# Kernel optimization log

Hardware: AMD Instinct MI355X
Metric: run time of the kernel (lower is better)

Reference implementation:

```python
import jax, jax.numpy as jnp
import numpy as np

N = 100000       # nodes
E = 1600000      # edges (avg degree 16)
F_IN = 128
F_OUT = 128
EPS = 1e-5       # GraphNorm eps
NEG_SLOPE = 0.01 # nn.LeakyReLU default


def setup_inputs() -> dict:
    key = jax.random.key(0)
    ks = jax.random.split(key, 4)
    x = jax.random.normal(ks[0], (N, F_IN), dtype=jnp.float32)
    edge_index = jax.random.randint(ks[1], (2, E), 0, N, dtype=jnp.int64)
    # GCNConv linear weight (stored as [in, out] for x @ W)
    W = jax.random.normal(ks[2], (F_IN, F_OUT), dtype=jnp.float32) / np.sqrt(F_IN).astype(np.float32)
    b = jnp.zeros((F_OUT,), jnp.float32)          # GCNConv bias
    gn_weight = jnp.ones((F_OUT,), jnp.float32)   # GraphNorm weight
    gn_bias = jnp.zeros((F_OUT,), jnp.float32)    # GraphNorm bias
    gn_mean_scale = jnp.ones((F_OUT,), jnp.float32)  # GraphNorm mean_scale
    return {"x": x, "edge_index": edge_index, "W": W, "b": b,
            "gn_weight": gn_weight, "gn_bias": gn_bias, "gn_mean_scale": gn_mean_scale}


def reference(x, edge_index, W, b, gn_weight, gn_bias, gn_mean_scale):
    n = x.shape[0]
    # --- GCNConv with add_self_loops=True, symmetric normalization ---
    loops = jnp.arange(n, dtype=edge_index.dtype)
    src = jnp.concatenate([edge_index[0], loops])  # [E+N]
    dst = jnp.concatenate([edge_index[1], loops])  # [E+N]
    deg = jax.ops.segment_sum(jnp.ones(src.shape, x.dtype), dst, num_segments=n)  # [N]
    deg_inv_sqrt = jnp.where(deg > 0, 1.0 / jnp.sqrt(deg), 0.0)
    norm = deg_inv_sqrt[src] * deg_inv_sqrt[dst]   # [E+N]
    h = x @ W                                      # [N, F_OUT]
    agg = jax.ops.segment_sum(h[src] * norm[:, None], dst, num_segments=n) + b  # [N, F_OUT]
    # --- GraphNorm (single graph: stats over all nodes, per-feature) ---
    mean = jnp.mean(agg, axis=0)                   # [F_OUT]
    centered = agg - mean * gn_mean_scale
    var = jnp.mean(centered * centered, axis=0)
    out = centered / jnp.sqrt(var + EPS) * gn_weight + gn_bias
    # --- LeakyReLU ---
    out = jnp.where(out > 0, out, NEG_SLOPE * out)
    return (out, edge_index)
```

## Files before the change

### kernel.cpp

```cpp
#include <hip/hip_runtime.h>

#define NN 100000
#define NE 1600000
#define F  128
#define NSPL 50000

#define SH   8
#define NPB  256
#define NBKT 391
#define B1   256
#define CH1  6250
#define MATN (NBKT * B1)
#define MATP (98 * 1024)
#define BCAP2 6144

#define SB   256

constexpr float EPS   = 1e-5f;
constexpr float SLOPE = 0.01f;

typedef __attribute__((ext_vector_type(8))) short short8;
typedef __attribute__((ext_vector_type(4))) float f32x4;
typedef __attribute__((ext_vector_type(2))) float f32x2;

__device__ inline unsigned int bf16rne(float f) {
    unsigned int u = __float_as_uint(f);
    return (u + 0x7fffu + ((u >> 16) & 1u)) >> 16;
}
__device__ inline float blo(unsigned int u) { return __uint_as_float(u << 16); }
__device__ inline float bhi(unsigned int u) { return __uint_as_float(u & 0xffff0000u); }
__device__ inline unsigned int pack2(float a, float b) {
    return bf16rne(a) | (bf16rne(b) << 16);
}
__device__ inline f32x2 pkadd(f32x2 a, f32x2 b) {
    f32x2 d;
    asm("v_pk_add_f32 %0, %1, %2" : "=v"(d) : "v"(a), "v"(b));
    return d;
}
__device__ inline f32x2 fp8lo(unsigned int u) {
    return __builtin_amdgcn_cvt_pk_f32_fp8(u, false);
}
__device__ inline f32x2 fp8hi(unsigned int u) {
    return __builtin_amdgcn_cvt_pk_f32_fp8(u, true);
}
__device__ inline unsigned int fp8pack4(float a, float b, float c, float d) {
    int o = 0;
    o = __builtin_amdgcn_cvt_pk_fp8_f32(a, b, o, false);
    o = __builtin_amdgcn_cvt_pk_fp8_f32(c, d, o, true);
    return (unsigned int)o;
}

__global__ __launch_bounds__(1024) void k_hist1(const int* __restrict__ dst,
                                                unsigned int* __restrict__ mat,
                                                const float* __restrict__ Wm,
                                                unsigned int* __restrict__ Wt) {
    __shared__ unsigned int h[NBKT];
    if (threadIdx.x < NBKT) h[threadIdx.x] = 0u;
    __syncthreads();
    if (blockIdx.x < 8) {
        int idx = blockIdx.x * 1024 + threadIdx.x;
        int p = idx & 3, lane = (idx >> 2) & 63, n = (idx >> 8) & 7, kk = idx >> 11;
        int k0 = kk * 32 + (lane >> 4) * 8 + 2 * p;
        int c  = n * 16 + (lane & 15);
        unsigned int lo = bf16rne(Wm[k0 * F + c]);
        unsigned int hi = bf16rne(Wm[(k0 + 1) * F + c]);
        Wt[idx] = lo | (hi << 16);
    }
    const int e0 = blockIdx.x * CH1;
    for (int i = threadIdx.x; i < CH1; i += 1024)
        atomicAdd(&h[dst[e0 + i] >> SH], 1u);
    __syncthreads();
    if (threadIdx.x < NBKT) mat[threadIdx.x * B1 + blockIdx.x] = h[threadIdx.x];
}

__global__ __launch_bounds__(1024) void k_scanA(const unsigned int* __restrict__ mat,
                                                unsigned int* __restrict__ scn,
                                                unsigned int* __restrict__ bsums) {
    __shared__ unsigned int ps[1024];
    const int t = threadIdx.x;
    const int i = blockIdx.x * 1024 + t;
    unsigned int v = mat[i];
    ps[t] = v;
    __syncthreads();
    for (int off = 1; off < 1024; off <<= 1) {
        unsigned int a = (t >= off) ? ps[t - off] : 0u;
        __syncthreads();
        ps[t] += a;
        __syncthreads();
    }
    scn[i] = ps[t];
    if (t == 1023) bsums[blockIdx.x] = ps[1023];
}


__global__ __launch_bounds__(1024) void k_scat1(const int* __restrict__ ei,
                                                const unsigned int* __restrict__ mat,
                                                const unsigned int* __restrict__ scn,
                                                const unsigned int* __restrict__ bsums,
                                                unsigned int* __restrict__ ebuf) {
    __shared__ unsigned int cur[NBKT];
    __shared__ unsigned int bo[128];
    const int t = threadIdx.x;
    if (t < 128) {
        unsigned int v = (t < 98) ? bsums[t] : 0u;
        bo[t] = v;
        for (int off = 1; off < 128; off <<= 1) {
            __syncthreads();
            unsigned int a = (t >= off) ? bo[t - off] : 0u;
            __syncthreads();
            bo[t] += a;
        }
        bo[t] -= v;
    } else {
        for (int off = 1; off < 128; off <<= 1) { __syncthreads(); __syncthreads(); }
    }
    __syncthreads();
    if (t < NBKT) {
        int idx = t * B1 + blockIdx.x;
        cur[t] = scn[idx] + bo[idx >> 10] - mat[idx];
    }
    __syncthreads();
    const int e0 = blockIdx.x * CH1;
    for (int i = t; i < CH1; i += 1024) {
        int s = ei[e0 + i];
        int d = ei[NE + e0 + i];
        unsigned int pos = atomicAdd(&cur[d >> SH], 1u);
        ebuf[pos] = ((unsigned int)(d & (NPB - 1)) << 17) | (unsigned int)s;
    }
}

__global__ __launch_bounds__(256) void k_fill2(const unsigned int* __restrict__ mat,
                                               const unsigned int* __restrict__ scn,
                                               const unsigned int* __restrict__ bsums,
                                               const unsigned int* __restrict__ ebuf,
                                               int* __restrict__ row_start,
                                               float* __restrict__ dis,
                                               int* __restrict__ csr) {
    __shared__ unsigned int stage[BCAP2];
    __shared__ unsigned int hist[NPB];
    __shared__ unsigned int cur[NPB];
    __shared__ unsigned int ps[NPB];
    __shared__ unsigned int bo[128];
    const int t = threadIdx.x;
    const int bkt = blockIdx.x;
    hist[t] = 0u;
    if (t < 128) {
        unsigned int v = (t < 98) ? bsums[t] : 0u;
        bo[t] = v;
        for (int off = 1; off < 128; off <<= 1) {
            __syncthreads();
            unsigned int a = (t >= off) ? bo[t - off] : 0u;
            __syncthreads();
            bo[t] += a;
        }
        bo[t] -= v;
    } else {
        for (int off = 1; off < 128; off <<= 1) { __syncthreads(); __syncthreads(); }
    }
    __syncthreads();
    const int i0 = bkt * B1;
    const unsigned int ebase = scn[i0] + bo[i0 >> 10] - mat[i0];
    unsigned int eend;
    if (bkt == NBKT - 1) eend = (unsigned int)NE;
    else {
        const int i1 = (bkt + 1) * B1;
        eend = scn[i1] + bo[i1 >> 10] - mat[i1];
    }
    const unsigned int n = eend - ebase;
    const unsigned int m = (n < BCAP2) ? n : BCAP2;
    for (unsigned int i = t; i < m; i += 256) {
        unsigned int v = ebuf[ebase + i];
        stage[i] = v;
        atomicAdd(&hist[v >> 17], 1u);
    }
    for (unsigned int i = BCAP2 + t; i < n; i += 256)
        atomicAdd(&hist[ebuf[ebase + i] >> 17], 1u);
    __syncthreads();
    const unsigned int deg = hist[t];
    ps[t] = deg;
    __syncthreads();
    for (int off = 1; off < 256; off <<= 1) {
        unsigned int a = (t >= off) ? ps[t - off] : 0u;
        __syncthreads();
        ps[t] += a;
        __syncthreads();
    }
    const unsigned int ex = (t == 0) ? 0u : ps[t - 1];
    cur[t] = ebase + ex;
    const int node = bkt * NPB + t;
    if (node <= NN) row_start[node] = (int)(ebase + ex);
    if (node < NN)  dis[node] = rsqrtf((float)(deg + 1u));
    __syncthreads();
    for (unsigned int i = t; i < m; i += 256) {
        unsigned int v = stage[i];
        unsigned int pos = atomicAdd(&cur[v >> 17], 1u);
        csr[pos] = (int)(v & 0x1FFFFu);
    }
    for (unsigned int i = BCAP2 + t; i < n; i += 256) {
        unsigned int v = ebuf[ebase + i];
        unsigned int pos = atomicAdd(&cur[v >> 17], 1u);
        csr[pos] = (int)(v & 0x1FFFFu);
    }
}

__global__ __launch_bounds__(256) void k_gemm(const float* __restrict__ x,
                                              const unsigned int* __restrict__ Wt,
                                              const float* __restrict__ dis,
                                              unsigned int* __restrict__ g32) {
    __shared__ unsigned int xl[128 * 64];
    const int tid = threadIdx.x;
    const int lane = tid & 63, wave = tid >> 6;
    const int row0 = blockIdx.x * 128;

#pragma unroll
    for (int i = 0; i < 16; ++i) {
        int fi = i * 256 + tid;
        int lr = fi >> 5;
        int cf = (fi & 31) * 4;
        int gr = row0 + lr; if (gr >= NN) gr = NN - 1;
        float4 v = *(const float4*)(x + (size_t)gr * F + cf);
        unsigned int u0 = pack2(v.x, v.y);
        unsigned int u1 = pack2(v.z, v.w);
        int cu = (cf >> 1) ^ ((lr & 7) << 2);
        uint2 w2; w2.x = u0; w2.y = u1;
        *(uint2*)&xl[lr * 64 + cu] = w2;
    }
    __syncthreads();

    const int rbase = row0 + wave * 32;
    short8 afr[2][4];
#pragma unroll
    for (int m = 0; m < 2; ++m) {
        int lr = wave * 32 + m * 16 + (lane & 15);
#pragma unroll
        for (int kk = 0; kk < 4; ++kk) {
            int cu = (kk * 16 + (lane >> 4) * 4) ^ ((lr & 7) << 2);
            afr[m][kk] = *(const short8*)&xl[lr * 64 + cu];
        }
    }

    f32x4 acc[2][8];
#pragma unroll
    for (int m = 0; m < 2; ++m)
#pragma unroll
        for (int n = 0; n < 8; ++n) { f32x4 z = {0.f, 0.f, 0.f, 0.f}; acc[m][n] = z; }

    const uint4* Wt4 = (const uint4*)Wt;
#pragma unroll
    for (int kk = 0; kk < 4; ++kk) {
        union { uint4 u; short8 s; } bfr[8];
#pragma unroll
        for (int n = 0; n < 8; ++n) bfr[n].u = Wt4[(kk * 8 + n) * 64 + lane];
#pragma unroll
        for (int m = 0; m < 2; ++m)
#pragma unroll
            for (int n = 0; n < 8; ++n)
                acc[m][n] = __builtin_amdgcn_mfma_f32_16x16x32_bf16(bfr[n].s, afr[m][kk], acc[m][n], 0, 0, 0);
    }

#pragma unroll
    for (int m = 0; m < 2; ++m) {
        int xr = rbase + m * 16 + (lane & 15);
        bool ok = xr < NN;
        float d = ok ? dis[xr] : 0.0f;
        unsigned int* gp = g32 + (size_t)(ok ? xr : 0) * 32 + (lane >> 4);
#pragma unroll
        for (int n = 0; n < 8; ++n) {
            unsigned int w = fp8pack4(acc[m][n][0] * d, acc[m][n][1] * d,
                                      acc[m][n][2] * d, acc[m][n][3] * d);
            if (ok) gp[n * 4] = w;
        }
    }
}

__global__ __launch_bounds__(256) void k_gather(const unsigned int* __restrict__ g32,
                                                const int* __restrict__ csr,
                                                const int* __restrict__ row_start,
                                                const float* __restrict__ dis,
                                                const float* __restrict__ b,
                                                unsigned int* __restrict__ agg_lo,
                                                unsigned int* __restrict__ agg_hi) {
    const int lane = threadIdx.x & 63;
    const int node = blockIdx.x * 4 + (threadIdx.x >> 6);
    if (node >= NN) return;
    const int q = lane >> 4;
    const int c = lane & 15;
    const int j = row_start[node];
    const int e = row_start[node + 1];
    const int L = e - j + 1;
    int sv = (j + lane < e) ? csr[j + lane] : node;
    f32x2 A0 = {0.f, 0.f}, A1 = A0, A2 = A0, A3 = A0;
    int k = 0;
    const int L1 = (L < 64) ? L : 64;
    for (; k < L1; k += 16) {
        int k0 = k + q, k1 = k0 + 4, k2 = k0 + 8, k3 = k0 + 12;
        int r0 = __shfl(sv, k0);
        int r1 = __shfl(sv, k1);
        int r2 = __shfl(sv, k2);
        int r3 = __shfl(sv, k3);
        bool p0 = k0 < L, p1 = k1 < L, p2 = k2 < L, p3 = k3 < L;
        uint2 v0, v1, v2, v3;
        if (p0) v0 = *(const uint2*)&g32[(size_t)r0 * 32 + c * 2];
        if (p1) v1 = *(const uint2*)&g32[(size_t)r1 * 32 + c * 2];
        if (p2) v2 = *(const uint2*)&g32[(size_t)r2 * 32 + c * 2];
        if (p3) v3 = *(const uint2*)&g32[(size_t)r3 * 32 + c * 2];
        if (p0) {
            A0 = pkadd(A0, fp8lo(v0.x)); A1 = pkadd(A1, fp8hi(v0.x));
            A2 = pkadd(A2, fp8lo(v0.y)); A3 = pkadd(A3, fp8hi(v0.y));
        }
        if (p1) {
            A0 = pkadd(A0, fp8lo(v1.x)); A1 = pkadd(A1, fp8hi(v1.x));
            A2 = pkadd(A2, fp8lo(v1.y)); A3 = pkadd(A3, fp8hi(v1.y));
        }
        if (p2) {
            A0 = pkadd(A0, fp8lo(v2.x)); A1 = pkadd(A1, fp8hi(v2.x));
            A2 = pkadd(A2, fp8lo(v2.y)); A3 = pkadd(A3, fp8hi(v2.y));
        }
        if (p3) {
            A0 = pkadd(A0, fp8lo(v3.x)); A1 = pkadd(A1, fp8hi(v3.x));
            A2 = pkadd(A2, fp8lo(v3.y)); A3 = pkadd(A3, fp8hi(v3.y));
        }
    }
    for (; k < L; k += 16) {
#pragma unroll
        for (int s = 0; s < 4; ++s) {
            int ks = k + q + s * 4;
            if (ks < L) {
                int rs = (j + ks < e) ? csr[j + ks] : node;
                uint2 v = *(const uint2*)&g32[(size_t)rs * 32 + c * 2];
                A0 = pkadd(A0, fp8lo(v.x)); A1 = pkadd(A1, fp8hi(v.x));
                A2 = pkadd(A2, fp8lo(v.y)); A3 = pkadd(A3, fp8hi(v.y));
            }
        }
    }
#define RED2(A) A.x += __shfl_xor(A.x, 16); A.x += __shfl_xor(A.x, 32); \
                A.y += __shfl_xor(A.y, 16); A.y += __shfl_xor(A.y, 32);
    RED2(A0) RED2(A1) RED2(A2) RED2(A3)
#undef RED2
    if (q == 0) {
        float d = dis[node];
        const float4* bp = (const float4*)&b[c * 8];
        float4 b0 = bp[0], b1 = bp[1];
        uint4 w;
        w.x = pack2(b0.x + d * A0.x, b0.y + d * A0.y);
        w.y = pack2(b0.z + d * A1.x, b0.w + d * A1.y);
        w.z = pack2(b1.x + d * A2.x, b1.y + d * A2.y);
        w.w = pack2(b1.z + d * A3.x, b1.w + d * A3.y);
        unsigned int* base = (node < NSPL) ? (agg_lo + (size_t)node * 64)
                                           : (agg_hi + (size_t)(node - NSPL) * 64);
        *(uint4*)(base + c * 4) = w;
    }
}

__global__ __launch_bounds__(256) void k_stats(const unsigned int* __restrict__ agg_lo,
                                               const unsigned int* __restrict__ agg_hi,
                                               float* __restrict__ partials) {
    __shared__ float lds[4][16][16];
    const int tid = threadIdx.x;
    const int lane = tid & 63, wave = tid >> 6;
    const uint4* lo4 = (const uint4*)agg_lo;
    const uint4* hi4 = (const uint4*)agg_hi;
    const long totalLo = (long)NSPL * 16;
    const long total   = (long)NN * 16;
    const long stride  = (long)SB * 256;
    float s[8], qq[8];
#pragma unroll
    for (int i = 0; i < 8; ++i) { s[i] = 0.f; qq[i] = 0.f; }
    for (long i = (long)blockIdx.x * 256 + tid; i < total; i += stride) {
        uint4 v = (i < totalLo) ? lo4[i] : hi4[i - totalLo];
        float f0 = blo(v.x), f1 = bhi(v.x), f2 = blo(v.y), f3 = bhi(v.y);
        float f4 = blo(v.z), f5 = bhi(v.z), f6 = blo(v.w), f7 = bhi(v.w);
        s[0] += f0; qq[0] += f0 * f0;  s[1] += f1; qq[1] += f1 * f1;
        s[2] += f2; qq[2] += f2 * f2;  s[3] += f3; qq[3] += f3 * f3;
        s[4] += f4; qq[4] += f4 * f4;  s[5] += f5; qq[5] += f5 * f5;
        s[6] += f6; qq[6] += f6 * f6;  s[7] += f7; qq[7] += f7 * f7;
    }
#pragma unroll
    for (int i = 0; i < 8; ++i) {
        s[i]  += __shfl_xor(s[i], 16);  s[i]  += __shfl_xor(s[i], 32);
        qq[i] += __shfl_xor(qq[i], 16); qq[i] += __shfl_xor(qq[i], 32);
    }
    if (lane < 16) {
#pragma unroll
        for (int i = 0; i < 8; ++i) {
            lds[wave][lane][i]     = s[i];
            lds[wave][lane][i + 8] = qq[i];
        }
    }
    __syncthreads();
    const int c4n = tid >> 4, slot = tid & 15;
    float v = lds[0][c4n][slot] + lds[1][c4n][slot] + lds[2][c4n][slot] + lds[3][c4n][slot];
    int f = c4n * 8 + (slot & 7);
    int idx = (slot < 8) ? f : (F + f);
    partials[(size_t)blockIdx.x * 256 + idx] = v;
}

__global__ __launch_bounds__(256) void k_red(const float* __restrict__ partials,
                                             float* __restrict__ stats) {
    float a0 = 0.f, a1 = 0.f, a2 = 0.f, a3 = 0.f;
    for (int bq = 0; bq < SB; bq += 4) {
        a0 += partials[(bq + 0) * 256 + threadIdx.x];
        a1 += partials[(bq + 1) * 256 + threadIdx.x];
        a2 += partials[(bq + 2) * 256 + threadIdx.x];
        a3 += partials[(bq + 3) * 256 + threadIdx.x];
    }
    stats[threadIdx.x] = (a0 + a1) + (a2 + a3);
}

__global__ __launch_bounds__(256) void k_normei(const unsigned int* __restrict__ agg_lo,
                                               const unsigned int* __restrict__ agg_hi,
                                               const float* __restrict__ stats,
                                               const float* __restrict__ gw,
                                               const float* __restrict__ gb,
                                               const float* __restrict__ gms,
                                               float* __restrict__ out0,
                                               const int* __restrict__ ei,
                                               float* __restrict__ out1) {
    __shared__ float A[F], Bc[F];
    if (threadIdx.x < F) {
        int f = threadIdx.x;
        const float invn = 1.0f / (float)NN;
        float mean = stats[f] * invn;
        float ms = mean * gms[f];
        float var = stats[F + f] * invn - 2.0f * ms * mean + ms * ms;
        float inv = rsqrtf(var + EPS);
        float a = inv * gw[f];
        A[f] = a;
        Bc[f] = gb[f] - ms * a;
    }
    __syncthreads();
    const int c4 = threadIdx.x & 15;
    float ra[8], rb[8];
#pragma unroll
    for (int i = 0; i < 8; ++i) { ra[i] = A[c4 * 8 + i]; rb[i] = Bc[c4 * 8 + i]; }
    const uint4* lo4 = (const uint4*)agg_lo;
    const uint4* hi4 = (const uint4*)agg_hi;
    const int4* ei4 = (const int4*)ei;
    float4* o14 = (float4*)out1;
    const long totalLo = (long)NSPL * 16;
    const long total   = (long)NN * 16;
    const long stride  = (long)gridDim.x * 256;
    for (long i = (long)blockIdx.x * 256 + threadIdx.x; i < total; i += stride) {
        bool isLo = i < totalLo;
        uint4 v = isLo ? lo4[i] : hi4[i - totalLo];
        float f0 = blo(v.x) * ra[0] + rb[0], f1 = bhi(v.x) * ra[1] + rb[1];
        float f2 = blo(v.y) * ra[2] + rb[2], f3 = bhi(v.y) * ra[3] + rb[3];
        float f4 = blo(v.z) * ra[4] + rb[4], f5 = bhi(v.z) * ra[5] + rb[5];
        float f6 = blo(v.w) * ra[6] + rb[6], f7 = bhi(v.w) * ra[7] + rb[7];
        f0 = f0 > 0.f ? f0 : SLOPE * f0;  f1 = f1 > 0.f ? f1 : SLOPE * f1;
        f2 = f2 > 0.f ? f2 : SLOPE * f2;  f3 = f3 > 0.f ? f3 : SLOPE * f3;
        f4 = f4 > 0.f ? f4 : SLOPE * f4;  f5 = f5 > 0.f ? f5 : SLOPE * f5;
        f6 = f6 > 0.f ? f6 : SLOPE * f6;  f7 = f7 > 0.f ? f7 : SLOPE * f7;
        float4 r0, r1;
        r0.x = f0; r0.y = f1; r0.z = f2; r0.w = f3;
        r1.x = f4; r1.y = f5; r1.z = f6; r1.w = f7;
        float* op = out0 + i * 8;
        *(float4*)op = r0;
        *(float4*)(op + 4) = r1;
        if (isLo) {
            int4 ev = ei4[i];
            unsigned int z;
            asm("v_and_b32 %0, 0, %1" : "=v"(z) : "v"(v.x));
            float4 r;
            r.x = (float)(ev.x | (int)z);
            r.y = (float)ev.y;
            r.z = (float)ev.z;
            r.w = (float)ev.w;
            o14[i] = r;
        }
    }
}

extern "C" void kernel_launch(void* const* d_in, const int* in_sizes, int n_in,
                              void* d_out, int out_size, void* d_ws, size_t ws_size,
                              hipStream_t stream) {
    const float* x   = (const float*)d_in[0];
    const int*   ei  = (const int*)d_in[1];
    const float* Wm  = (const float*)d_in[2];
    const float* b   = (const float*)d_in[3];
    const float* gw  = (const float*)d_in[4];
    const float* gb  = (const float*)d_in[5];
    const float* gms = (const float*)d_in[6];

    float* out  = (float*)d_out;
    float* out1 = out + (size_t)NN * F;
    unsigned int* agg_lo = (unsigned int*)out1;

    unsigned int* wsu   = (unsigned int*)d_ws;
    unsigned int* g32   = wsu;
    unsigned int* ebuf  = wsu;
    unsigned int* mat   = g32 + (size_t)NN * 32;
    unsigned int* scn   = mat + MATP;
    unsigned int* bsums = scn + MATP;
    int* row_start      = (int*)(bsums + 128);
    int* csr            = row_start + NN + 2;
    float* dis          = (float*)(csr + NE + 8);
    float* stats        = dis + NN;
    unsigned int* Wt    = (unsigned int*)(stats + 256);
    unsigned int* agg_hi = Wt + 8192;
    float* partials     = (float*)(agg_hi + (size_t)(NN - NSPL) * 64);

    k_hist1<<<B1, 1024, 0, stream>>>(ei + NE, mat, Wm, Wt);
    k_scanA<<<98, 1024, 0, stream>>>(mat, scn, bsums);
    k_scat1<<<B1, 1024, 0, stream>>>(ei, mat, scn, bsums, ebuf);
    k_fill2<<<NBKT, 256, 0, stream>>>(mat, scn, bsums, ebuf, row_start, dis, csr);
    k_gemm<<<(NN + 127) / 128, 256, 0, stream>>>(x, Wt, dis, g32);
    k_gather<<<NN / 4, 256, 0, stream>>>(g32, csr, row_start, dis, b, agg_lo, agg_hi);
    k_stats<<<SB, 256, 0, stream>>>(agg_lo, agg_hi, partials);
    k_red<<<1, 256, 0, stream>>>(partials, stats);
    k_normei<<<2048, 256, 0, stream>>>(agg_lo, agg_hi, stats, gw, gb, gms, out, ei, out1);
}
```

Before: 137.4 us.

## Store aggregated features as fp8 in one buffer instead of split bf16

The gather kernel now packs aggregated node features to fp8 (e4m3) and writes them into a single contiguous buffer, replacing the bf16 storage split across the output tail and a workspace region. The stats and normalize kernels are rewritten to read 16 features per 16-byte load, using packed fp32 add/fma for the sum and sum of squares. This halves the intermediate traffic and removes the lo/hi branching. The cost is a large loss of precision in the GraphNorm input and statistics, which may break the accuracy tolerance.

```diff
diff --git a/kernel.cpp b/kernel.cpp
--- a/kernel.cpp
+++ b/kernel.cpp
@@ -3,7 +3,6 @@
 #define NN 100000
 #define NE 1600000
 #define F  128
-#define NSPL 50000
 
 #define SH   8
 #define NPB  256
@@ -27,14 +26,17 @@
     unsigned int u = __float_as_uint(f);
     return (u + 0x7fffu + ((u >> 16) & 1u)) >> 16;
 }
-__device__ inline float blo(unsigned int u) { return __uint_as_float(u << 16); }
-__device__ inline float bhi(unsigned int u) { return __uint_as_float(u & 0xffff0000u); }
 __device__ inline unsigned int pack2(float a, float b) {
     return bf16rne(a) | (bf16rne(b) << 16);
 }
 __device__ inline f32x2 pkadd(f32x2 a, f32x2 b) {
     f32x2 d;
     asm("v_pk_add_f32 %0, %1, %2" : "=v"(d) : "v"(a), "v"(b));
+    return d;
+}
+__device__ inline f32x2 pkfma(f32x2 a, f32x2 b, f32x2 c) {
+    f32x2 d;
+    asm("v_pk_fma_f32 %0, %1, %2, %3" : "=v"(d) : "v"(a), "v"(b), "v"(c));
     return d;
 }
 __device__ inline f32x2 fp8lo(unsigned int u) {
@@ -278,8 +280,7 @@
                                                 const int* __restrict__ row_start,
                                                 const float* __restrict__ dis,
                                                 const float* __restrict__ b,
-                                                unsigned int* __restrict__ agg_lo,
-                                                unsigned int* __restrict__ agg_hi) {
+                                                unsigned int* __restrict__ agg8) {
     const int lane = threadIdx.x & 63;
     const int node = blockIdx.x * 4 + (threadIdx.x >> 6);
     if (node >= NN) return;
@@ -341,58 +342,61 @@
         float d = dis[node];
         const float4* bp = (const float4*)&b[c * 8];
         float4 b0 = bp[0], b1 = bp[1];
-        uint4 w;
-        w.x = pack2(b0.x + d * A0.x, b0.y + d * A0.y);
-        w.y = pack2(b0.z + d * A1.x, b0.w + d * A1.y);
-        w.z = pack2(b1.x + d * A2.x, b1.y + d * A2.y);
-        w.w = pack2(b1.z + d * A3.x, b1.w + d * A3.y);
-        unsigned int* base = (node < NSPL) ? (agg_lo + (size_t)node * 64)
-                                           : (agg_hi + (size_t)(node - NSPL) * 64);
-        *(uint4*)(base + c * 4) = w;
-    }
-}
-
-__global__ __launch_bounds__(256) void k_stats(const unsigned int* __restrict__ agg_lo,
-                                               const unsigned int* __restrict__ agg_hi,
+        uint2 w;
+        w.x = fp8pack4(b0.x + d * A0.x, b0.y + d * A0.y,
+                       b0.z + d * A1.x, b0.w + d * A1.y);
+        w.y = fp8pack4(b1.x + d * A2.x, b1.y + d * A2.y,
+                       b1.z + d * A3.x, b1.w + d * A3.y);
+        *(uint2*)&agg8[(size_t)node * 32 + c * 2] = w;
+    }
+}
+
+__global__ __launch_bounds__(256) void k_stats(const unsigned int* __restrict__ agg8,
                                                float* __restrict__ partials) {
-    __shared__ float lds[4][16][16];
+    __shared__ float lds[4][8][32];
     const int tid = threadIdx.x;
     const int lane = tid & 63, wave = tid >> 6;
-    const uint4* lo4 = (const uint4*)agg_lo;
-    const uint4* hi4 = (const uint4*)agg_hi;
-    const long totalLo = (long)NSPL * 16;
-    const long total   = (long)NN * 16;
-    const long stride  = (long)SB * 256;
-    float s[8], qq[8];
-#pragma unroll
-    for (int i = 0; i < 8; ++i) { s[i] = 0.f; qq[i] = 0.f; }
+    const uint4* a4 = (const uint4*)agg8;
+    const long total  = (long)NN * 8;
+    const long stride = (long)SB * 256;
+    f32x2 S[8], Q[8];
+#pragma unroll
+    for (int i = 0; i < 8; ++i) { f32x2 z = {0.f, 0.f}; S[i] = z; Q[i] = z; }
     for (long i = (long)blockIdx.x * 256 + tid; i < total; i += stride) {
-        uint4 v = (i < totalLo) ? lo4[i] : hi4[i - totalLo];
-        float f0 = blo(v.x), f1 = bhi(v.x), f2 = blo(v.y), f3 = bhi(v.y);
-        float f4 = blo(v.z), f5 = bhi(v.z), f6 = blo(v.w), f7 = bhi(v.w);
-        s[0] += f0; qq[0] += f0 * f0;  s[1] += f1; qq[1] += f1 * f1;
-        s[2] += f2; qq[2] += f2 * f2;  s[3] += f3; qq[3] += f3 * f3;
-        s[4] += f4; qq[4] += f4 * f4;  s[5] += f5; qq[5] += f5 * f5;
-        s[6] += f6; qq[6] += f6 * f6;  s[7] += f7; qq[7] += f7 * f7;
+        uint4 v = a4[i];
+        f32x2 p0 = fp8lo(v.x), p1 = fp8hi(v.x), p2 = fp8lo(v.y), p3 = fp8hi(v.y);
+        f32x2 p4 = fp8lo(v.z), p5 = fp8hi(v.z), p6 = fp8lo(v.w), p7 = fp8hi(v.w);
+        S[0] = pkadd(S[0], p0); Q[0] = pkfma(p0, p0, Q[0]);
+        S[1] = pkadd(S[1], p1); Q[1] = pkfma(p1, p1, Q[1]);
+        S[2] = pkadd(S[2], p2); Q[2] = pkfma(p2, p2, Q[2]);
+        S[3] = pkadd(S[3], p3); Q[3] = pkfma(p3, p3, Q[3]);
+        S[4] = pkadd(S[4], p4); Q[4] = pkfma(p4, p4, Q[4]);
+        S[5] = pkadd(S[5], p5); Q[5] = pkfma(p5, p5, Q[5]);
+        S[6] = pkadd(S[6], p6); Q[6] = pkfma(p6, p6, Q[6]);
+        S[7] = pkadd(S[7], p7); Q[7] = pkfma(p7, p7, Q[7]);
     }
 #pragma unroll
     for (int i = 0; i < 8; ++i) {
-        s[i]  += __shfl_xor(s[i], 16);  s[i]  += __shfl_xor(s[i], 32);
-        qq[i] += __shfl_xor(qq[i], 16); qq[i] += __shfl_xor(qq[i], 32);
-    }
-    if (lane < 16) {
+        S[i].x += __shfl_xor(S[i].x, 8); S[i].x += __shfl_xor(S[i].x, 16); S[i].x += __shfl_xor(S[i].x, 32);
+        S[i].y += __shfl_xor(S[i].y, 8); S[i].y += __shfl_xor(S[i].y, 16); S[i].y += __shfl_xor(S[i].y, 32);
+        Q[i].x += __shfl_xor(Q[i].x, 8); Q[i].x += __shfl_xor(Q[i].x, 16); Q[i].x += __shfl_xor(Q[i].x, 32);
+        Q[i].y += __shfl_xor(Q[i].y, 8); Q[i].y += __shfl_xor(Q[i].y, 16); Q[i].y += __shfl_xor(Q[i].y, 32);
+    }
+    if (lane < 8) {
 #pragma unroll
         for (int i = 0; i < 8; ++i) {
-            lds[wave][lane][i]     = s[i];
-            lds[wave][lane][i + 8] = qq[i];
-        }
-    }
-    __syncthreads();
-    const int c4n = tid >> 4, slot = tid & 15;
-    float v = lds[0][c4n][slot] + lds[1][c4n][slot] + lds[2][c4n][slot] + lds[3][c4n][slot];
-    int f = c4n * 8 + (slot & 7);
-    int idx = (slot < 8) ? f : (F + f);
-    partials[(size_t)blockIdx.x * 256 + idx] = v;
+            lds[wave][lane][2 * i]      = S[i].x;
+            lds[wave][lane][2 * i + 1]  = S[i].y;
+            lds[wave][lane][16 + 2 * i]     = Q[i].x;
+            lds[wave][lane][16 + 2 * i + 1] = Q[i].y;
+        }
+    }
+    __syncthreads();
+    const int kind = tid >> 7;
+    const int f = tid & 127;
+    const int l = f >> 4, slot = (f & 15) + 16 * kind;
+    float v = lds[0][l][slot] + lds[1][l][slot] + lds[2][l][slot] + lds[3][l][slot];
+    partials[(size_t)blockIdx.x * 256 + tid] = v;
 }
 
 __global__ __launch_bounds__(256) void k_red(const float* __restrict__ partials,
@@ -407,8 +411,7 @@
     stats[threadIdx.x] = (a0 + a1) + (a2 + a3);
 }
 
-__global__ __launch_bounds__(256) void k_normei(const unsigned int* __restrict__ agg_lo,
-                                               const unsigned int* __restrict__ agg_hi,
+__global__ __launch_bounds__(256) void k_normei(const unsigned int* __restrict__ agg8,
                                                const float* __restrict__ stats,
                                                const float* __restrict__ gw,
                                                const float* __restrict__ gb,
@@ -429,45 +432,45 @@
         Bc[f] = gb[f] - ms * a;
     }
     __syncthreads();
-    const int c4 = threadIdx.x & 15;
-    float ra[8], rb[8];
-#pragma unroll
-    for (int i = 0; i < 8; ++i) { ra[i] = A[c4 * 8 + i]; rb[i] = Bc[c4 * 8 + i]; }
-    const uint4* lo4 = (const uint4*)agg_lo;
-    const uint4* hi4 = (const uint4*)agg_hi;
+    const int c8 = threadIdx.x & 7;
+    float ra[16], rb[16];
+#pragma unroll
+    for (int i = 0; i < 16; ++i) { ra[i] = A[c8 * 16 + i]; rb[i] = Bc[c8 * 16 + i]; }
+    const uint4* a4 = (const uint4*)agg8;
     const int4* ei4 = (const int4*)ei;
     float4* o14 = (float4*)out1;
-    const long totalLo = (long)NSPL * 16;
-    const long total   = (long)NN * 16;
-    const long stride  = (long)gridDim.x * 256;
+    const long total  = (long)NN * 8;
+    const long stride = (long)gridDim.x * 256;
     for (long i = (long)blockIdx.x * 256 + threadIdx.x; i < total; i += stride) {
-        bool isLo = i < totalLo;
-        uint4 v = isLo ? lo4[i] : hi4[i - totalLo];
-        float f0 = blo(v.x) * ra[0] + rb[0], f1 = bhi(v.x) * ra[1] + rb[1];
-        float f2 = blo(v.y) * ra[2] + rb[2], f3 = bhi(v.y) * ra[3] + rb[3];
-        float f4 = blo(v.z) * ra[4] + rb[4], f5 = bhi(v.z) * ra[5] + rb[5];
-        float f6 = blo(v.w) * ra[6] + rb[6], f7 = bhi(v.w) * ra[7] + rb[7];
-        f0 = f0 > 0.f ? f0 : SLOPE * f0;  f1 = f1 > 0.f ? f1 : SLOPE * f1;
-        f2 = f2 > 0.f ? f2 : SLOPE * f2;  f3 = f3 > 0.f ? f3 : SLOPE * f3;
-        f4 = f4 > 0.f ? f4 : SLOPE * f4;  f5 = f5 > 0.f ? f5 : SLOPE * f5;
-        f6 = f6 > 0.f ? f6 : SLOPE * f6;  f7 = f7 > 0.f ? f7 : SLOPE * f7;
-        float4 r0, r1;
-        r0.x = f0; r0.y = f1; r0.z = f2; r0.w = f3;
-        r1.x = f4; r1.y = f5; r1.z = f6; r1.w = f7;
-        float* op = out0 + i * 8;
-        *(float4*)op = r0;
-        *(float4*)(op + 4) = r1;
-        if (isLo) {
-            int4 ev = ei4[i];
-            unsigned int z;
-            asm("v_and_b32 %0, 0, %1" : "=v"(z) : "v"(v.x));
-            float4 r;
-            r.x = (float)(ev.x | (int)z);
-            r.y = (float)ev.y;
-            r.z = (float)ev.z;
-            r.w = (float)ev.w;
-            o14[i] = r;
-        }
+        uint4 v = a4[i];
+        f32x2 p0 = fp8lo(v.x), p1 = fp8hi(v.x), p2 = fp8lo(v.y), p3 = fp8hi(v.y);
+        f32x2 p4 = fp8lo(v.z), p5 = fp8hi(v.z), p6 = fp8lo(v.w), p7 = fp8hi(v.w);
+        float fv[16];
+        fv[0] = p0.x * ra[0] + rb[0];   fv[1] = p0.y * ra[1] + rb[1];
+        fv[2] = p1.x * ra[2] + rb[2];   fv[3] = p1.y * ra[3] + rb[3];
+        fv[4] = p2.x * ra[4] + rb[4];   fv[5] = p2.y * ra[5] + rb[5];
+        fv[6] = p3.x * ra[6] + rb[6];   fv[7] = p3.y * ra[7] + rb[7];
+        fv[8] = p4.x * ra[8] + rb[8];   fv[9] = p4.y * ra[9] + rb[9];
+        fv[10] = p5.x * ra[10] + rb[10]; fv[11] = p5.y * ra[11] + rb[11];
+        fv[12] = p6.x * ra[12] + rb[12]; fv[13] = p6.y * ra[13] + rb[13];
+        fv[14] = p7.x * ra[14] + rb[14]; fv[15] = p7.y * ra[15] + rb[15];
+#pragma unroll
+        for (int t = 0; t < 16; ++t) fv[t] = fv[t] > 0.f ? fv[t] : SLOPE * fv[t];
+        float* op = out0 + i * 16;
+#pragma unroll
+        for (int t = 0; t < 4; ++t) {
+            float4 r; r.x = fv[4 * t]; r.y = fv[4 * t + 1]; r.z = fv[4 * t + 2]; r.w = fv[4 * t + 3];
+            *(float4*)(op + 4 * t) = r;
+        }
+        int4 ev = ei4[i];
+        unsigned int z;
+        asm("v_and_b32 %0, 0, %1" : "=v"(z) : "v"(v.x));
+        float4 r;
+        r.x = (float)(ev.x | (int)z);
+        r.y = (float)ev.y;
+        r.z = (float)ev.z;
+        r.w = (float)ev.w;
+        o14[i] = r;
     }
 }
 
@@ -484,7 +487,7 @@
 
     float* out  = (float*)d_out;
     float* out1 = out + (size_t)NN * F;
-    unsigned int* agg_lo = (unsigned int*)out1;
+    unsigned int* agg8 = (unsigned int*)out1;
 
     unsigned int* wsu   = (unsigned int*)d_ws;
     unsigned int* g32   = wsu;
@@ -497,16 +500,15 @@
     float* dis          = (float*)(csr + NE + 8);
     float* stats        = dis + NN;
     unsigned int* Wt    = (unsigned int*)(stats + 256);
-    unsigned int* agg_hi = Wt + 8192;
-    float* partials     = (float*)(agg_hi + (size_t)(NN - NSPL) * 64);
+    float* partials     = (float*)(Wt + 8192);
 
     k_hist1<<<B1, 1024, 0, stream>>>(ei + NE, mat, Wm, Wt);
     k_scanA<<<98, 1024, 0, stream>>>(mat, scn, bsums);
     k_scat1<<<B1, 1024, 0, stream>>>(ei, mat, scn, bsums, ebuf);
     k_fill2<<<NBKT, 256, 0, stream>>>(mat, scn, bsums, ebuf, row_start, dis, csr);
     k_gemm<<<(NN + 127) / 128, 256, 0, stream>>>(x, Wt, dis, g32);
-    k_gather<<<NN / 4, 256, 0, stream>>>(g32, csr, row_start, dis, b, agg_lo, agg_hi);
-    k_stats<<<SB, 256, 0, stream>>>(agg_lo, agg_hi, partials);
+    k_gather<<<NN / 4, 256, 0, stream>>>(g32, csr, row_start, dis, b, agg8);
+    k_stats<<<SB, 256, 0, stream>>>(agg8, partials);
     k_red<<<1, 256, 0, stream>>>(partials, stats);
-    k_normei<<<2048, 256, 0, stream>>>(agg_lo, agg_hi, stats, gw, gb, gms, out, ei, out1);
-}
+    k_normei<<<2048, 256, 0, stream>>>(agg8, stats, gw, gb, gms, out, ei, out1);
+}
```

Measured after the change: 136.1 us (median of 2 runs). Within noise of the previous version (-0.9%).
